# Performance work log

Measured on AMD Instinct MI355X. Metric: run time of the kernel, lower is better.

The kernel has to match this reference:

```python
import jax, jax.numpy as jnp
import numpy as np

N_NODES = 100000
N_EDGES = 800000
F_IN = 128
H1, C1 = 8, 32
N_CLS = 40
NEG_SLOPE = 0.2


def setup_inputs() -> dict:
    key = jax.random.key(0)
    ks = jax.random.split(key, 10)
    s = 1.0 / np.sqrt(F_IN)
    s2 = 1.0 / np.sqrt(H1 * C1)
    return {
        "x": jax.random.normal(ks[0], (N_NODES, F_IN), jnp.float32),
        "edge_index": jax.random.randint(ks[1], (2, N_EDGES), 0, N_NODES, jnp.int64),
        "W1": jax.random.normal(ks[2], (F_IN, H1 * C1), jnp.float32) * s,
        "a_src1": jax.random.normal(ks[3], (H1, C1), jnp.float32) * s2,
        "a_dst1": jax.random.normal(ks[4], (H1, C1), jnp.float32) * s2,
        "b1": jnp.zeros((H1 * C1,), jnp.float32),
        "W2": jax.random.normal(ks[5], (H1 * C1, N_CLS), jnp.float32) * s2,
        "a_src2": jax.random.normal(ks[6], (1, N_CLS), jnp.float32) * 0.1,
        "a_dst2": jax.random.normal(ks[7], (1, N_CLS), jnp.float32) * 0.1,
        "b2": jnp.zeros((N_CLS,), jnp.float32),
    }


def gat_conv(x, src, dst, W, a_src, a_dst, b, heads, out_ch, concat):
    n = x.shape[0]
    h = (x @ W).reshape(n, heads, out_ch)            # [N,H,C]
    alpha_s = jnp.einsum("nhc,hc->nh", h, a_src)     # [N,H]
    alpha_d = jnp.einsum("nhc,hc->nh", h, a_dst)
    e = alpha_s[src] + alpha_d[dst]                  # [E,H]
    e = jax.nn.leaky_relu(e, NEG_SLOPE)
    # per-destination segment softmax (stable)
    m = jax.ops.segment_max(e, dst, num_segments=n)  # [N,H]
    e = jnp.exp(e - m[dst])
    denom = jax.ops.segment_sum(e, dst, num_segments=n)
    alpha = e / (denom[dst] + 1e-16)                 # [E,H]
    msg = alpha[:, :, None] * h[src]                 # [E,H,C]
    out = jax.ops.segment_sum(msg, dst, num_segments=n)  # [N,H,C]
    out = out.reshape(n, heads * out_ch) if concat else out.mean(axis=1)
    return out + b


def reference(x, edge_index, W1, a_src1, a_dst1, b1, W2, a_src2, a_dst2, b2):
    n = x.shape[0]
    # PyG GATConv default add_self_loops=True
    loop = jnp.arange(n, dtype=edge_index.dtype)
    src = jnp.concatenate([edge_index[0], loop])
    dst = jnp.concatenate([edge_index[1], loop])
    # dropout layers are identity in eval mode
    h = gat_conv(x, src, dst, W1, a_src1, a_dst1, b1, H1, C1, concat=True)
    h = jax.nn.elu(h)
    out = gat_conv(h, src, dst, W2, a_src2, a_dst2, b2, 1, N_CLS, concat=False)
    return jax.nn.log_softmax(out, axis=1)
```

## Files before the change

kernel.cpp:

```cpp
#include <hip/hip_runtime.h>
#include <hip/hip_fp16.h>
#include <math.h>

#define N_NODESc 100000
#define N_EDGESc 800000
#define F_INc    128
#define HC1c     256
#define NCLSc    40
#define NEG_SLOPEc 0.2f
#define CAPc     40
#define CSH      4

typedef _Float16 half8 __attribute__((ext_vector_type(8)));
typedef __fp16   f16x2 __attribute__((ext_vector_type(2)));
typedef float    f32x4 __attribute__((ext_vector_type(4)));
typedef float    f32x2 __attribute__((ext_vector_type(2)));

__device__ __forceinline__ unsigned pack_ws(float w, int src) {
    union { f16x2 h; unsigned u; } t;
    t.h = __builtin_amdgcn_cvt_pkrtz(w, w);
    return (unsigned)src | ((t.u & 0xFFFFu) << 17);
}
__device__ __forceinline__ float unpack_w(unsigned pe) {
    union { unsigned short s; __fp16 h; } t;
    t.s = (unsigned short)(pe >> 17);
    return (float)t.h;
}


__global__ void k_init(const float* __restrict__ W1, const float* __restrict__ W2,
                       _Float16* __restrict__ W1Tf, _Float16* __restrict__ W2Tf,
                       int* __restrict__ cnt) {
    if (blockIdx.x < 22) {
        int f = blockIdx.x * 256 + threadIdx.x;
        if (f < 4096) {
            int lane16 = f & 15, quad = (f >> 4) & 3, k0 = (f >> 6) & 3, jt = f >> 8;
            int c = lane16 * 16 + jt;
            int kbase = k0 * 32 + quad * 8;
            _Float16* o = W1Tf + (size_t)f * 8;
            #pragma unroll
            for (int j = 0; j < 8; j++) o[j] = (_Float16)W1[(kbase + j) * HC1c + c];
        } else if (f < 4096 + 1536) {
            int g = f - 4096;
            int lane16 = g & 15, quad = (g >> 4) & 3, k0 = (g >> 6) & 7, jt = g >> 9;
            int c = jt * 16 + lane16;
            int kbase = k0 * 32 + quad * 8;
            _Float16* o = W2Tf + (size_t)g * 8;
            #pragma unroll
            for (int j = 0; j < 8; j++)
                o[j] = (c < NCLSc) ? (_Float16)W2[(kbase + j) * NCLSc + c] : (_Float16)0.f;
        }
    } else {
        int i = (blockIdx.x - 22) * 256 + threadIdx.x;
        if (i < N_NODESc * 4) ((int4*)cnt)[i] = (int4){0, 0, 0, 0};
    }
}


__global__ __launch_bounds__(256) void k_gemm1_scatter(
    const float* __restrict__ x, const _Float16* __restrict__ W1Tf,
    const float* __restrict__ a_src1, const float* __restrict__ a_dst1,
    unsigned char* __restrict__ h1f8, float* __restrict__ as1, float* __restrict__ ad1,
    const int* __restrict__ src, const int* __restrict__ dst,
    int* __restrict__ cnt, int* __restrict__ bucket) {
    if ((blockIdx.x & 1) == 0) {
        int i = (blockIdx.x >> 1) * 256 + threadIdx.x;
        if (i < N_EDGESc / 4) {
            int4 s = ((const int4*)src)[i];
            int4 d = ((const int4*)dst)[i];
            int p0 = atomicAdd(&cnt[d.x << CSH], 1);
            if (p0 < CAPc) __builtin_nontemporal_store(s.x, &bucket[d.x * CAPc + p0]);
            int p1 = atomicAdd(&cnt[d.y << CSH], 1);
            if (p1 < CAPc) __builtin_nontemporal_store(s.y, &bucket[d.y * CAPc + p1]);
            int p2 = atomicAdd(&cnt[d.z << CSH], 1);
            if (p2 < CAPc) __builtin_nontemporal_store(s.z, &bucket[d.z * CAPc + p2]);
            int p3 = atomicAdd(&cnt[d.w << CSH], 1);
            if (p3 < CAPc) __builtin_nontemporal_store(s.w, &bucket[d.w * CAPc + p3]);
        }
        return;
    }
    int wave = ((blockIdx.x >> 1) * 256 + threadIdx.x) >> 6;
    int n0 = wave * 16;
    if (n0 >= N_NODESc) return;
    int L = threadIdx.x & 63, lane16 = L & 15, quad = L >> 4;
    f32x4 acc[16];
    #pragma unroll
    for (int jt = 0; jt < 16; jt++) acc[jt] = (f32x4){0.f, 0.f, 0.f, 0.f};
    const float* A = x + (size_t)(n0 + lane16) * F_INc + quad * 8;
    const _Float16* Bf = W1Tf + L * 8;
    #pragma unroll
    for (int k0 = 0; k0 < 4; k0++) {
        float4 f0 = *(const float4*)(A + k0 * 32);
        float4 f1 = *(const float4*)(A + k0 * 32 + 4);
        union { half8 v; f16x2 h[4]; } af;
        af.h[0] = __builtin_amdgcn_cvt_pkrtz(f0.x, f0.y);
        af.h[1] = __builtin_amdgcn_cvt_pkrtz(f0.z, f0.w);
        af.h[2] = __builtin_amdgcn_cvt_pkrtz(f1.x, f1.y);
        af.h[3] = __builtin_amdgcn_cvt_pkrtz(f1.z, f1.w);
        #pragma unroll
        for (int jt = 0; jt < 16; jt++) {
            half8 bf = *(const half8*)(Bf + (jt * 4 + k0) * 512);
            acc[jt] = __builtin_amdgcn_mfma_f32_16x16x32_f16(af.v, bf, acc[jt], 0, 0, 0);
        }
    }
    {
        #pragma unroll
        for (int r = 0; r < 4; r++) {
            uint4 st;
            int d;
            d = __builtin_amdgcn_cvt_pk_fp8_f32(acc[0][r], acc[1][r], 0, false);
            d = __builtin_amdgcn_cvt_pk_fp8_f32(acc[2][r], acc[3][r], d, true);
            st.x = (unsigned)d;
            d = __builtin_amdgcn_cvt_pk_fp8_f32(acc[4][r], acc[5][r], 0, false);
            d = __builtin_amdgcn_cvt_pk_fp8_f32(acc[6][r], acc[7][r], d, true);
            st.y = (unsigned)d;
            d = __builtin_amdgcn_cvt_pk_fp8_f32(acc[8][r], acc[9][r], 0, false);
            d = __builtin_amdgcn_cvt_pk_fp8_f32(acc[10][r], acc[11][r], d, true);
            st.z = (unsigned)d;
            d = __builtin_amdgcn_cvt_pk_fp8_f32(acc[12][r], acc[13][r], 0, false);
            d = __builtin_amdgcn_cvt_pk_fp8_f32(acc[14][r], acc[15][r], d, true);
            st.w = (unsigned)d;
            *(uint4*)(h1f8 + (size_t)(n0 + quad * 4 + r) * HC1c + lane16 * 16) = st;
        }
    }
    {
        float asv[16], adv[16];
        const float4* ap = (const float4*)(a_src1 + lane16 * 16);
        const float4* dp = (const float4*)(a_dst1 + lane16 * 16);
        #pragma unroll
        for (int q = 0; q < 4; q++) {
            float4 a4 = ap[q], d4 = dp[q];
            asv[4*q] = a4.x; asv[4*q+1] = a4.y; asv[4*q+2] = a4.z; asv[4*q+3] = a4.w;
            adv[4*q] = d4.x; adv[4*q+1] = d4.y; adv[4*q+2] = d4.z; adv[4*q+3] = d4.w;
        }
        float ps[4] = {0,0,0,0}, pd[4] = {0,0,0,0};
        #pragma unroll
        for (int jt = 0; jt < 16; jt++) {
            #pragma unroll
            for (int r = 0; r < 4; r++) {
                ps[r] += acc[jt][r] * asv[jt];
                pd[r] += acc[jt][r] * adv[jt];
            }
        }
        #pragma unroll
        for (int r = 0; r < 4; r++) {
            ps[r] += __shfl_xor(ps[r], 1);
            pd[r] += __shfl_xor(pd[r], 1);
        }
        if ((lane16 & 1) == 0) {
            int h = lane16 >> 1;
            #pragma unroll
            for (int r = 0; r < 4; r++) {
                int n = n0 + quad * 4 + r;
                as1[n * 8 + h] = ps[r];
                ad1[n * 8 + h] = pd[r];
            }
        }
    }
}


__global__ __launch_bounds__(256) void k_agg1(
    const int* __restrict__ cnt, const int* __restrict__ bucket,
    const float* __restrict__ as1, const float* __restrict__ ad1,
    const unsigned char* __restrict__ h1f8, const float* __restrict__ b1,
    _Float16* __restrict__ act1b) {
    int n = blockIdx.x * 4 + (threadIdx.x >> 6);
    if (n >= N_NODESc) return;
    int L = threadIdx.x & 63;
    int eL = L >> 3, hL = L & 7;
    int hA = L >> 3;
    int beg = n * CAPc;
    int end = beg + min(cnt[n << CSH], CAPc);
    float ad = ad1[n * 8 + hL];
    float vs = as1[n * 8 + hL] + ad;
    float s_self = (vs > 0.f) ? vs : NEG_SLOPEc * vs;
    float m_run = s_self, d_run = 1.f;
    unsigned ldself = *((const unsigned*)(h1f8 + (size_t)n * HC1c) + L);
    f32x2 accA = __builtin_amdgcn_cvt_pk_f32_fp8((int)ldself, false);
    f32x2 accB = __builtin_amdgcn_cvt_pk_f32_fp8((int)ldself, true);
    for (int base = beg; base < end; base += 16) {
        int m = min(16, end - base);
        int src0 = 0, src1 = 0;
        float s0 = -INFINITY, s1 = -INFINITY;
        if (eL < m) {
            src0 = bucket[base + eL];
            float v = as1[src0 * 8 + hL] + ad;
            s0 = (v > 0.f) ? v : NEG_SLOPEc * v;
        }
        if (eL + 8 < m) {
            src1 = bucket[base + eL + 8];
            float v = as1[src1 * 8 + hL] + ad;
            s1 = (v > 0.f) ? v : NEG_SLOPEc * v;
        }
        float mc = fmaxf(s0, s1);
        mc = fmaxf(mc, __shfl_xor(mc, 8));
        mc = fmaxf(mc, __shfl_xor(mc, 16));
        mc = fmaxf(mc, __shfl_xor(mc, 32));
        float mnew = fmaxf(m_run, mc);
        float w0 = (eL < m) ? __expf(s0 - mnew) : 0.f;
        float w1 = (eL + 8 < m) ? __expf(s1 - mnew) : 0.f;
        float wsum = w0 + w1;
        wsum += __shfl_xor(wsum, 8);
        wsum += __shfl_xor(wsum, 16);
        wsum += __shfl_xor(wsum, 32);
        float scale = __expf(m_run - mnew);
        d_run = d_run * scale + wsum;
        m_run = mnew;
        float sc = __shfl(scale, hA);
        f32x2 sc2 = (f32x2){sc, sc};
        accA *= sc2;
        accB *= sc2;
        unsigned pk0 = pack_ws(w0, src0);
        unsigned pk1 = pack_ws(w1, src1);
        #pragma unroll
        for (int r = 0; r < 4; r++) {
            int e0 = r * 4;
            if (e0 < m) {
                unsigned pk = (e0 < 8) ? pk0 : pk1;
                unsigned pe[4]; unsigned ld[4];
                #pragma unroll
                for (int j = 0; j < 4; j++)
                    pe[j] = __shfl(pk, ((e0 + j) & 7) * 8 + hA);
                #pragma unroll
                for (int j = 0; j < 4; j++)
                    ld[j] = *((const unsigned*)(h1f8 + (size_t)(pe[j] & 0x1FFFFu) * HC1c) + L);
                #pragma unroll
                for (int j = 0; j < 4; j++) {
                    float w = unpack_w(pe[j]);
                    f32x2 wv = (f32x2){w, w};
                    f32x2 lo = __builtin_amdgcn_cvt_pk_f32_fp8((int)ld[j], false);
                    f32x2 hi = __builtin_amdgcn_cvt_pk_f32_fp8((int)ld[j], true);
                    asm("v_pk_fma_f32 %0, %1, %2, %0" : "+v"(accA) : "v"(wv), "v"(lo));
                    asm("v_pk_fma_f32 %0, %1, %2, %0" : "+v"(accB) : "v"(wv), "v"(hi));
                }
            }
        }
    }
    float inv = __builtin_amdgcn_rcpf(d_run + 1e-16f);
    float inv_h = __shfl(inv, hA);
    float4 bb = ((const float4*)b1)[L];
    float o0 = accA[0] * inv_h + bb.x;
    float o1 = accA[1] * inv_h + bb.y;
    float o2 = accB[0] * inv_h + bb.z;
    float o3 = accB[1] * inv_h + bb.w;
    o0 = (o0 > 0.f) ? o0 : (__expf(o0) - 1.f);
    o1 = (o1 > 0.f) ? o1 : (__expf(o1) - 1.f);
    o2 = (o2 > 0.f) ? o2 : (__expf(o2) - 1.f);
    o3 = (o3 > 0.f) ? o3 : (__expf(o3) - 1.f);
    union { uint2 u; f16x2 h[2]; } st;
    st.h[0] = __builtin_amdgcn_cvt_pkrtz(o0, o1);
    st.h[1] = __builtin_amdgcn_cvt_pkrtz(o2, o3);
    ((uint2*)(act1b + (size_t)n * HC1c))[L] = st.u;
}


__global__ __launch_bounds__(256) void k_gemm2(
    const _Float16* __restrict__ act1b, const _Float16* __restrict__ W2Tf,
    const float* __restrict__ a_src2, const float* __restrict__ a_dst2,
    _Float16* __restrict__ h2b, float* __restrict__ as2, float* __restrict__ ad2) {
    int wave = (blockIdx.x * 256 + threadIdx.x) >> 6;
    int n0 = wave * 16;
    if (n0 >= N_NODESc) return;
    int L = threadIdx.x & 63, lane16 = L & 15, quad = L >> 4;
    f32x4 acc[3];
    #pragma unroll
    for (int jt = 0; jt < 3; jt++) acc[jt] = (f32x4){0.f, 0.f, 0.f, 0.f};
    const _Float16* A = act1b + (size_t)(n0 + lane16) * HC1c + quad * 8;
    const _Float16* Bf = W2Tf + L * 8;
    #pragma unroll
    for (int k0 = 0; k0 < 8; k0++) {
        half8 af = *(const half8*)(A + k0 * 32);
        #pragma unroll
        for (int jt = 0; jt < 3; jt++) {
            half8 bf = *(const half8*)(Bf + (jt * 8 + k0) * 512);
            acc[jt] = __builtin_amdgcn_mfma_f32_16x16x32_f16(af, bf, acc[jt], 0, 0, 0);
        }
    }
    float ps[4] = {0.f, 0.f, 0.f, 0.f}, pd[4] = {0.f, 0.f, 0.f, 0.f};
    #pragma unroll
    for (int jt = 0; jt < 3; jt++) {
        int col = jt * 16 + lane16;
        float ws = (col < NCLSc) ? a_src2[col] : 0.f;
        float wd = (col < NCLSc) ? a_dst2[col] : 0.f;
        #pragma unroll
        for (int r = 0; r < 4; r++) {
            float v = acc[jt][r];
            int n = n0 + quad * 4 + r;
            if (col < NCLSc) h2b[(size_t)n * NCLSc + col] = (_Float16)v;
            ps[r] += v * ws; pd[r] += v * wd;
        }
    }
    #pragma unroll
    for (int r = 0; r < 4; r++) {
        float s = ps[r], d = pd[r];
        s += __shfl_xor(s, 1); d += __shfl_xor(d, 1);
        s += __shfl_xor(s, 2); d += __shfl_xor(d, 2);
        s += __shfl_xor(s, 4); d += __shfl_xor(d, 4);
        s += __shfl_xor(s, 8); d += __shfl_xor(d, 8);
        if (lane16 == 0) {
            int n = n0 + quad * 4 + r;
            as2[n] = s; ad2[n] = d;
        }
    }
}


__global__ __launch_bounds__(256) void k_agg2(
    const int* __restrict__ cnt, const int* __restrict__ bucket,
    const float* __restrict__ as2, const float* __restrict__ ad2,
    const _Float16* __restrict__ h2b, const float* __restrict__ b2,
    float* __restrict__ out) {
    int n = blockIdx.x * 4 + (threadIdx.x >> 6);
    if (n >= N_NODESc) return;
    int L = threadIdx.x & 63;
    int g = L / 20, cls = L % 20;
    int beg = n * CAPc;
    int end = beg + min(cnt[n << CSH], CAPc);
    float ad = ad2[n];
    float vs = as2[n] + ad;
    float s_self = (vs > 0.f) ? vs : NEG_SLOPEc * vs;
    float m_run = s_self, d_run = 1.f;
    f16x2 acc2 = (f16x2){(__fp16)0.f, (__fp16)0.f};
    if (g == 0) {
        union { unsigned u; f16x2 h; } pk;
        pk.u = *((const unsigned*)(h2b + (size_t)n * NCLSc) + cls);
        acc2 = pk.h;
    }
    for (int base = beg; base < end; base += 64) {
        int m = min(64, end - base);
        int src = 0; float s = -INFINITY;
        if (L < m) {
            src = bucket[base + L];
            float v = as2[src] + ad;
            s = (v > 0.f) ? v : NEG_SLOPEc * v;
        }
        float mc = s;
        for (int o = 32; o; o >>= 1) mc = fmaxf(mc, __shfl_xor(mc, o));
        float mnew = fmaxf(m_run, mc);
        float w = (L < m) ? __expf(s - mnew) : 0.f;
        float ws = w;
        for (int o = 32; o; o >>= 1) ws += __shfl_xor(ws, o);
        float scale = __expf(m_run - mnew);
        d_run = d_run * scale + ws;
        m_run = mnew;
        f16x2 sc2 = __builtin_amdgcn_cvt_pkrtz(scale, scale);
        acc2 *= sc2;
        for (int jb = 0; jb < m; jb += 9) {
            float wv[3]; int sev[3]; unsigned ldv[3];
            #pragma unroll
            for (int r = 0; r < 3; r++) {
                int e = jb + r * 3 + g;
                int lane = (e < 64) ? e : 63;
                wv[r] = __shfl(w, lane);
                sev[r] = __shfl(src, lane);
            }
            #pragma unroll
            for (int r = 0; r < 3; r++) {
                ldv[r] = 0u;
                if (g < 3)
                    ldv[r] = *((const unsigned*)(h2b + (size_t)sev[r] * NCLSc) + cls);
            }
            #pragma unroll
            for (int r = 0; r < 3; r++) {
                f16x2 we2 = __builtin_amdgcn_cvt_pkrtz(wv[r], wv[r]);
                union { unsigned u; f16x2 h; } pk; pk.u = ldv[r];
                acc2 += we2 * pk.h;
            }
        }
    }
    union { f16x2 h; int i; } au; au.h = acc2;
    int i1 = __shfl(au.i, (L + 20) & 63);
    int i2 = __shfl(au.i, (L + 40) & 63);
    union { int i; f16x2 h; } b1u, b2u; b1u.i = i1; b2u.i = i2;
    acc2 = acc2 + b1u.h + b2u.h;
    float vx = -INFINITY, vy = -INFINITY;
    if (L < 20) {
        float2 bb = ((const float2*)b2)[L];
        float inv = __builtin_amdgcn_rcpf(d_run + 1e-16f);
        vx = (float)acc2[0] * inv + bb.x;
        vy = (float)acc2[1] * inv + bb.y;
    }
    float mv = fmaxf(vx, vy);
    for (int o = 32; o; o >>= 1) mv = fmaxf(mv, __shfl_xor(mv, o));
    float ex = (L < 20) ? __expf(vx - mv) + __expf(vy - mv) : 0.f;
    for (int o = 32; o; o >>= 1) ex += __shfl_xor(ex, o);
    float ls = __logf(ex);
    if (L < 20) {
        float2 o2; o2.x = vx - mv - ls; o2.y = vy - mv - ls;
        ((float2*)(out + (size_t)n * NCLSc))[L] = o2;
    }
}


extern "C" void kernel_launch(void* const* d_in, const int* in_sizes, int n_in,
                              void* d_out, int out_size, void* d_ws, size_t ws_size,
                              hipStream_t stream) {
    const float* x    = (const float*)d_in[0];
    const int*   ei   = (const int*)d_in[1];
    const float* W1   = (const float*)d_in[2];
    const float* as1w = (const float*)d_in[3];
    const float* ad1w = (const float*)d_in[4];
    const float* b1   = (const float*)d_in[5];
    const float* W2   = (const float*)d_in[6];
    const float* as2w = (const float*)d_in[7];
    const float* ad2w = (const float*)d_in[8];
    const float* b2   = (const float*)d_in[9];
    float* out = (float*)d_out;

    char* p = (char*)d_ws;
    unsigned char* h1f8 = (unsigned char*)p; p += (size_t)N_NODESc * HC1c;
    _Float16* act1b = (_Float16*)p; p += (size_t)N_NODESc * HC1c * 2;
    _Float16* W1Tf  = (_Float16*)p; p += (size_t)4096 * 8 * 2;
    _Float16* W2Tf  = (_Float16*)p; p += (size_t)1536 * 8 * 2;
    float* a_s1 = (float*)p; p += (size_t)N_NODESc * 8 * 4;
    float* a_d1 = (float*)p; p += (size_t)N_NODESc * 8 * 4;
    _Float16* h2b = (_Float16*)p; p += (size_t)N_NODESc * NCLSc * 2;
    float* a_s2 = (float*)p; p += (size_t)N_NODESc * 4;
    float* a_d2 = (float*)p; p += (size_t)N_NODESc * 4;
    int* cnt    = (int*)p;   p += (size_t)N_NODESc * 16 * 4;
    int* bucket = (int*)p;   p += (size_t)N_NODESc * CAPc * 4;
    (void)ws_size; (void)in_sizes; (void)n_in; (void)out_size;

    const int* src = ei;
    const int* dst = ei + N_EDGESc;

    k_init<<<22 + (N_NODESc * 4 + 255) / 256, 256, 0, stream>>>(W1, W2, W1Tf, W2Tf, cnt);

    int nwave_blk = ((N_NODESc + 15) / 16 + 3) / 4;
    k_gemm1_scatter<<<nwave_blk * 2, 256, 0, stream>>>(
        x, W1Tf, as1w, ad1w, h1f8, a_s1, a_d1, src, dst, cnt, bucket);

    k_agg1<<<(N_NODESc + 3) / 4, 256, 0, stream>>>(cnt, bucket, a_s1, a_d1, h1f8, b1, act1b);
    k_gemm2<<<nwave_blk, 256, 0, stream>>>(act1b, W2Tf, as2w, ad2w, h2b, a_s2, a_d2);
    k_agg2<<<(N_NODESc + 3) / 4, 256, 0, stream>>>(cnt, bucket, a_s2, a_d2, h2b, b2, out);
}
```

Baseline: 292.8 us.

## Fuse layer-1 aggregation with layer-2 GEMM through shared memory and interleave scatter blocks

Merges the layer-1 aggregation kernel and the layer-2 GEMM kernel. Each block aggregates 16 nodes (4 per wave), writes the ELU activations as fp16 into swizzled LDS, and then one wave runs the MFMA GEMM against W2. This removes the 51 MB fp16 act1b round trip through global memory and one kernel launch, at the cost of idle waves during the GEMM phase and a block-wide barrier. The gemm1/scatter kernel also changes its block mapping from alternating single blocks to groups of 8, which alters how edge-scatter and GEMM work are interleaved.

Result: slower. 301.0 us (+2.8%).

```diff
diff --git a/kernel.cpp b/kernel.cpp
--- a/kernel.cpp
+++ b/kernel.cpp
@@ -63,8 +63,10 @@
     unsigned char* __restrict__ h1f8, float* __restrict__ as1, float* __restrict__ ad1,
     const int* __restrict__ src, const int* __restrict__ dst,
     int* __restrict__ cnt, int* __restrict__ bucket) {
-    if ((blockIdx.x & 1) == 0) {
-        int i = (blockIdx.x >> 1) * 256 + threadIdx.x;
+    int grp = blockIdx.x >> 3, within = blockIdx.x & 7;
+    if ((grp & 1) == 0) {
+        int sb = (grp >> 1) * 8 + within;
+        int i = sb * 256 + threadIdx.x;
         if (i < N_EDGESc / 4) {
             int4 s = ((const int4*)src)[i];
             int4 d = ((const int4*)dst)[i];
@@ -79,7 +81,8 @@
         }
         return;
     }
-    int wave = ((blockIdx.x >> 1) * 256 + threadIdx.x) >> 6;
+    int gb = (grp >> 1) * 8 + within;
+    int wave = (gb * 256 + (int)threadIdx.x) >> 6;
     int n0 = wave * 16;
     if (n0 >= N_NODESc) return;
     int L = threadIdx.x & 63, lane16 = L & 15, quad = L >> 4;
@@ -160,147 +163,150 @@
 }
 
 
-__global__ __launch_bounds__(256) void k_agg1(
+__global__ __launch_bounds__(256) void k_agg1_g2(
     const int* __restrict__ cnt, const int* __restrict__ bucket,
     const float* __restrict__ as1, const float* __restrict__ ad1,
     const unsigned char* __restrict__ h1f8, const float* __restrict__ b1,
-    _Float16* __restrict__ act1b) {
-    int n = blockIdx.x * 4 + (threadIdx.x >> 6);
-    if (n >= N_NODESc) return;
+    const _Float16* __restrict__ W2Tf, const float* __restrict__ a_src2,
+    const float* __restrict__ a_dst2, _Float16* __restrict__ h2b,
+    float* __restrict__ as2, float* __restrict__ ad2) {
+    __shared__ _Float16 sact[16 * HC1c];
     int L = threadIdx.x & 63;
+    int wid = threadIdx.x >> 6;
     int eL = L >> 3, hL = L & 7;
     int hA = L >> 3;
-    int beg = n * CAPc;
-    int end = beg + min(cnt[n << CSH], CAPc);
-    float ad = ad1[n * 8 + hL];
-    float vs = as1[n * 8 + hL] + ad;
-    float s_self = (vs > 0.f) ? vs : NEG_SLOPEc * vs;
-    float m_run = s_self, d_run = 1.f;
-    unsigned ldself = *((const unsigned*)(h1f8 + (size_t)n * HC1c) + L);
-    f32x2 accA = __builtin_amdgcn_cvt_pk_f32_fp8((int)ldself, false);
-    f32x2 accB = __builtin_amdgcn_cvt_pk_f32_fp8((int)ldself, true);
-    for (int base = beg; base < end; base += 16) {
-        int m = min(16, end - base);
-        int src0 = 0, src1 = 0;
-        float s0 = -INFINITY, s1 = -INFINITY;
-        if (eL < m) {
-            src0 = bucket[base + eL];
-            float v = as1[src0 * 8 + hL] + ad;
-            s0 = (v > 0.f) ? v : NEG_SLOPEc * v;
-        }
-        if (eL + 8 < m) {
-            src1 = bucket[base + eL + 8];
-            float v = as1[src1 * 8 + hL] + ad;
-            s1 = (v > 0.f) ? v : NEG_SLOPEc * v;
-        }
-        float mc = fmaxf(s0, s1);
-        mc = fmaxf(mc, __shfl_xor(mc, 8));
-        mc = fmaxf(mc, __shfl_xor(mc, 16));
-        mc = fmaxf(mc, __shfl_xor(mc, 32));
-        float mnew = fmaxf(m_run, mc);
-        float w0 = (eL < m) ? __expf(s0 - mnew) : 0.f;
-        float w1 = (eL + 8 < m) ? __expf(s1 - mnew) : 0.f;
-        float wsum = w0 + w1;
-        wsum += __shfl_xor(wsum, 8);
-        wsum += __shfl_xor(wsum, 16);
-        wsum += __shfl_xor(wsum, 32);
-        float scale = __expf(m_run - mnew);
-        d_run = d_run * scale + wsum;
-        m_run = mnew;
-        float sc = __shfl(scale, hA);
-        f32x2 sc2 = (f32x2){sc, sc};
-        accA *= sc2;
-        accB *= sc2;
-        unsigned pk0 = pack_ws(w0, src0);
-        unsigned pk1 = pack_ws(w1, src1);
+    float4 bb = ((const float4*)b1)[L];
+    #pragma unroll 1
+    for (int nn = 0; nn < 4; nn++) {
+        int row = wid * 4 + nn;
+        int n = blockIdx.x * 16 + row;
+        int beg = n * CAPc;
+        int end = beg + min(cnt[n << CSH], CAPc);
+        float ad = ad1[n * 8 + hL];
+        float vs = as1[n * 8 + hL] + ad;
+        float s_self = (vs > 0.f) ? vs : NEG_SLOPEc * vs;
+        float m_run = s_self, d_run = 1.f;
+        unsigned ldself = *((const unsigned*)(h1f8 + (size_t)n * HC1c) + L);
+        f32x2 accA = __builtin_amdgcn_cvt_pk_f32_fp8((int)ldself, false);
+        f32x2 accB = __builtin_amdgcn_cvt_pk_f32_fp8((int)ldself, true);
+        for (int base = beg; base < end; base += 16) {
+            int m = min(16, end - base);
+            int src0 = 0, src1 = 0;
+            float s0 = -INFINITY, s1 = -INFINITY;
+            if (eL < m) {
+                src0 = bucket[base + eL];
+                float v = as1[src0 * 8 + hL] + ad;
+                s0 = (v > 0.f) ? v : NEG_SLOPEc * v;
+            }
+            if (eL + 8 < m) {
+                src1 = bucket[base + eL + 8];
+                float v = as1[src1 * 8 + hL] + ad;
+                s1 = (v > 0.f) ? v : NEG_SLOPEc * v;
+            }
+            float mc = fmaxf(s0, s1);
+            mc = fmaxf(mc, __shfl_xor(mc, 8));
+            mc = fmaxf(mc, __shfl_xor(mc, 16));
+            mc = fmaxf(mc, __shfl_xor(mc, 32));
+            float mnew = fmaxf(m_run, mc);
+            float w0 = (eL < m) ? __expf(s0 - mnew) : 0.f;
+            float w1 = (eL + 8 < m) ? __expf(s1 - mnew) : 0.f;
+            float wsum = w0 + w1;
+            wsum += __shfl_xor(wsum, 8);
+            wsum += __shfl_xor(wsum, 16);
+            wsum += __shfl_xor(wsum, 32);
+            float scale = __expf(m_run - mnew);
+            d_run = d_run * scale + wsum;
+            m_run = mnew;
+            float sc = __shfl(scale, hA);
+            f32x2 sc2 = (f32x2){sc, sc};
+            accA *= sc2;
+            accB *= sc2;
+            unsigned pk0 = pack_ws(w0, src0);
+            unsigned pk1 = pack_ws(w1, src1);
+            #pragma unroll
+            for (int r = 0; r < 4; r++) {
+                int e0 = r * 4;
+                if (e0 < m) {
+                    unsigned pk = (e0 < 8) ? pk0 : pk1;
+                    unsigned pe[4]; unsigned ld[4];
+                    #pragma unroll
+                    for (int j = 0; j < 4; j++)
+                        pe[j] = __shfl(pk, ((e0 + j) & 7) * 8 + hA);
+                    #pragma unroll
+                    for (int j = 0; j < 4; j++)
+                        ld[j] = *((const unsigned*)(h1f8 + (size_t)(pe[j] & 0x1FFFFu) * HC1c) + L);
+                    #pragma unroll
+                    for (int j = 0; j < 4; j++) {
+                        float w = unpack_w(pe[j]);
+                        f32x2 wv = (f32x2){w, w};
+                        f32x2 lo = __builtin_amdgcn_cvt_pk_f32_fp8((int)ld[j], false);
+                        f32x2 hi = __builtin_amdgcn_cvt_pk_f32_fp8((int)ld[j], true);
+                        asm("v_pk_fma_f32 %0, %1, %2, %0" : "+v"(accA) : "v"(wv), "v"(lo));
+                        asm("v_pk_fma_f32 %0, %1, %2, %0" : "+v"(accB) : "v"(wv), "v"(hi));
+                    }
+                }
+            }
+        }
+        float inv = __builtin_amdgcn_rcpf(d_run + 1e-16f);
+        float inv_h = __shfl(inv, hA);
+        float o0 = accA[0] * inv_h + bb.x;
+        float o1 = accA[1] * inv_h + bb.y;
+        float o2 = accB[0] * inv_h + bb.z;
+        float o3 = accB[1] * inv_h + bb.w;
+        o0 = (o0 > 0.f) ? o0 : (__expf(o0) - 1.f);
+        o1 = (o1 > 0.f) ? o1 : (__expf(o1) - 1.f);
+        o2 = (o2 > 0.f) ? o2 : (__expf(o2) - 1.f);
+        o3 = (o3 > 0.f) ? o3 : (__expf(o3) - 1.f);
+        union { uint2 u; f16x2 h[2]; } st;
+        st.h[0] = __builtin_amdgcn_cvt_pkrtz(o0, o1);
+        st.h[1] = __builtin_amdgcn_cvt_pkrtz(o2, o3);
+        unsigned bofs = ((unsigned)(row * 512 + L * 8)) ^ ((unsigned)(row & 7) << 4);
+        *(uint2*)((char*)sact + bofs) = st.u;
+    }
+    __syncthreads();
+    if (threadIdx.x < 64) {
+        int lane16 = L & 15, quad = L >> 4;
+        int n0 = blockIdx.x * 16;
+        f32x4 acc[3];
+        #pragma unroll
+        for (int jt = 0; jt < 3; jt++) acc[jt] = (f32x4){0.f, 0.f, 0.f, 0.f};
+        const _Float16* Bf = W2Tf + L * 8;
+        unsigned rmask = ((unsigned)(lane16 & 7) << 4);
+        #pragma unroll
+        for (int k0 = 0; k0 < 8; k0++) {
+            unsigned abofs = ((unsigned)(lane16 * 512 + quad * 16 + k0 * 64)) ^ rmask;
+            half8 af = *(const half8*)((const char*)sact + abofs);
+            #pragma unroll
+            for (int jt = 0; jt < 3; jt++) {
+                half8 bf = *(const half8*)(Bf + (jt * 8 + k0) * 512);
+                acc[jt] = __builtin_amdgcn_mfma_f32_16x16x32_f16(af, bf, acc[jt], 0, 0, 0);
+            }
+        }
+        float ps[4] = {0.f, 0.f, 0.f, 0.f}, pd[4] = {0.f, 0.f, 0.f, 0.f};
+        #pragma unroll
+        for (int jt = 0; jt < 3; jt++) {
+            int col = jt * 16 + lane16;
+            float ws = (col < NCLSc) ? a_src2[col] : 0.f;
+            float wd = (col < NCLSc) ? a_dst2[col] : 0.f;
+            #pragma unroll
+            for (int r = 0; r < 4; r++) {
+                float v = acc[jt][r];
+                int n = n0 + quad * 4 + r;
+                if (col < NCLSc) h2b[(size_t)n * NCLSc + col] = (_Float16)v;
+                ps[r] += v * ws; pd[r] += v * wd;
+            }
+        }
         #pragma unroll
         for (int r = 0; r < 4; r++) {
-            int e0 = r * 4;
-            if (e0 < m) {
-                unsigned pk = (e0 < 8) ? pk0 : pk1;
-                unsigned pe[4]; unsigned ld[4];
-                #pragma unroll
-                for (int j = 0; j < 4; j++)
-                    pe[j] = __shfl(pk, ((e0 + j) & 7) * 8 + hA);
-                #pragma unroll
-                for (int j = 0; j < 4; j++)
-                    ld[j] = *((const unsigned*)(h1f8 + (size_t)(pe[j] & 0x1FFFFu) * HC1c) + L);
-                #pragma unroll
-                for (int j = 0; j < 4; j++) {
-                    float w = unpack_w(pe[j]);
-                    f32x2 wv = (f32x2){w, w};
-                    f32x2 lo = __builtin_amdgcn_cvt_pk_f32_fp8((int)ld[j], false);
-                    f32x2 hi = __builtin_amdgcn_cvt_pk_f32_fp8((int)ld[j], true);
-                    asm("v_pk_fma_f32 %0, %1, %2, %0" : "+v"(accA) : "v"(wv), "v"(lo));
-                    asm("v_pk_fma_f32 %0, %1, %2, %0" : "+v"(accB) : "v"(wv), "v"(hi));
-                }
-            }
-        }
-    }
-    float inv = __builtin_amdgcn_rcpf(d_run + 1e-16f);
-    float inv_h = __shfl(inv, hA);
-    float4 bb = ((const float4*)b1)[L];
-    float o0 = accA[0] * inv_h + bb.x;
-    float o1 = accA[1] * inv_h + bb.y;
-    float o2 = accB[0] * inv_h + bb.z;
-    float o3 = accB[1] * inv_h + bb.w;
-    o0 = (o0 > 0.f) ? o0 : (__expf(o0) - 1.f);
-    o1 = (o1 > 0.f) ? o1 : (__expf(o1) - 1.f);
-    o2 = (o2 > 0.f) ? o2 : (__expf(o2) - 1.f);
-    o3 = (o3 > 0.f) ? o3 : (__expf(o3) - 1.f);
-    union { uint2 u; f16x2 h[2]; } st;
-    st.h[0] = __builtin_amdgcn_cvt_pkrtz(o0, o1);
-    st.h[1] = __builtin_amdgcn_cvt_pkrtz(o2, o3);
-    ((uint2*)(act1b + (size_t)n * HC1c))[L] = st.u;
-}
-
-
-__global__ __launch_bounds__(256) void k_gemm2(
-    const _Float16* __restrict__ act1b, const _Float16* __restrict__ W2Tf,
-    const float* __restrict__ a_src2, const float* __restrict__ a_dst2,
-    _Float16* __restrict__ h2b, float* __restrict__ as2, float* __restrict__ ad2) {
-    int wave = (blockIdx.x * 256 + threadIdx.x) >> 6;
-    int n0 = wave * 16;
-    if (n0 >= N_NODESc) return;
-    int L = threadIdx.x & 63, lane16 = L & 15, quad = L >> 4;
-    f32x4 acc[3];
-    #pragma unroll
-    for (int jt = 0; jt < 3; jt++) acc[jt] = (f32x4){0.f, 0.f, 0.f, 0.f};
-    const _Float16* A = act1b + (size_t)(n0 + lane16) * HC1c + quad * 8;
-    const _Float16* Bf = W2Tf + L * 8;
-    #pragma unroll
-    for (int k0 = 0; k0 < 8; k0++) {
-        half8 af = *(const half8*)(A + k0 * 32);
-        #pragma unroll
-        for (int jt = 0; jt < 3; jt++) {
-            half8 bf = *(const half8*)(Bf + (jt * 8 + k0) * 512);
-            acc[jt] = __builtin_amdgcn_mfma_f32_16x16x32_f16(af, bf, acc[jt], 0, 0, 0);
-        }
-    }
-    float ps[4] = {0.f, 0.f, 0.f, 0.f}, pd[4] = {0.f, 0.f, 0.f, 0.f};
-    #pragma unroll
-    for (int jt = 0; jt < 3; jt++) {
-        int col = jt * 16 + lane16;
-        float ws = (col < NCLSc) ? a_src2[col] : 0.f;
-        float wd = (col < NCLSc) ? a_dst2[col] : 0.f;
-        #pragma unroll
-        for (int r = 0; r < 4; r++) {
-            float v = acc[jt][r];
-            int n = n0 + quad * 4 + r;
-            if (col < NCLSc) h2b[(size_t)n * NCLSc + col] = (_Float16)v;
-            ps[r] += v * ws; pd[r] += v * wd;
-        }
-    }
-    #pragma unroll
-    for (int r = 0; r < 4; r++) {
-        float s = ps[r], d = pd[r];
-        s += __shfl_xor(s, 1); d += __shfl_xor(d, 1);
-        s += __shfl_xor(s, 2); d += __shfl_xor(d, 2);
-        s += __shfl_xor(s, 4); d += __shfl_xor(d, 4);
-        s += __shfl_xor(s, 8); d += __shfl_xor(d, 8);
-        if (lane16 == 0) {
-            int n = n0 + quad * 4 + r;
-            as2[n] = s; ad2[n] = d;
+            float s = ps[r], d = pd[r];
+            s += __shfl_xor(s, 1); d += __shfl_xor(d, 1);
+            s += __shfl_xor(s, 2); d += __shfl_xor(d, 2);
+            s += __shfl_xor(s, 4); d += __shfl_xor(d, 4);
+            s += __shfl_xor(s, 8); d += __shfl_xor(d, 8);
+            if (lane16 == 0) {
+                int n = n0 + quad * 4 + r;
+                as2[n] = s; ad2[n] = d;
+            }
         }
     }
 }
@@ -410,7 +416,6 @@
 
     char* p = (char*)d_ws;
     unsigned char* h1f8 = (unsigned char*)p; p += (size_t)N_NODESc * HC1c;
-    _Float16* act1b = (_Float16*)p; p += (size_t)N_NODESc * HC1c * 2;
     _Float16* W1Tf  = (_Float16*)p; p += (size_t)4096 * 8 * 2;
     _Float16* W2Tf  = (_Float16*)p; p += (size_t)1536 * 8 * 2;
     float* a_s1 = (float*)p; p += (size_t)N_NODESc * 8 * 4;
@@ -427,11 +432,11 @@
 
     k_init<<<22 + (N_NODESc * 4 + 255) / 256, 256, 0, stream>>>(W1, W2, W1Tf, W2Tf, cnt);
 
-    int nwave_blk = ((N_NODESc + 15) / 16 + 3) / 4;
-    k_gemm1_scatter<<<nwave_blk * 2, 256, 0, stream>>>(
+    k_gemm1_scatter<<<3136, 256, 0, stream>>>(
         x, W1Tf, as1w, ad1w, h1f8, a_s1, a_d1, src, dst, cnt, bucket);
 
-    k_agg1<<<(N_NODESc + 3) / 4, 256, 0, stream>>>(cnt, bucket, a_s1, a_d1, h1f8, b1, act1b);
-    k_gemm2<<<nwave_blk, 256, 0, stream>>>(act1b, W2Tf, as2w, ad2w, h2b, a_s2, a_d2);
+    k_agg1_g2<<<N_NODESc / 16, 256, 0, stream>>>(
+        cnt, bucket, a_s1, a_d1, h1f8, b1, W2Tf, as2w, ad2w, h2b, a_s2, a_d2);
+
     k_agg2<<<(N_NODESc + 3) / 4, 256, 0, stream>>>(cnt, bucket, a_s2, a_d2, h2b, b2, out);
 }
```

## Process two destination nodes per wave in layer-2 aggregation

Applied to the files above, without the earlier changes.

The layer-2 aggregation kernel now gives each 64-lane wave two destination nodes, one per 32-lane half, instead of one node split into three 20-lane edge groups. Reductions shrink to 32-lane shuffles, the final cross-group combine goes away, and the grid is halved. The scatter phase also issues all four atomics before the bucket stores so their latencies overlap. Per-node edge parallelism drops from three edges per step to one (unrolled by three), which could lengthen the dependent load chain on high-degree nodes.

New measurement: 280.1 us. -4.4%, faster.

```diff
diff --git a/kernel.cpp b/kernel.cpp
--- a/kernel.cpp
+++ b/kernel.cpp
@@ -69,17 +69,17 @@
             int4 s = ((const int4*)src)[i];
             int4 d = ((const int4*)dst)[i];
             int p0 = atomicAdd(&cnt[d.x << CSH], 1);
+            int p1 = atomicAdd(&cnt[d.y << CSH], 1);
+            int p2 = atomicAdd(&cnt[d.z << CSH], 1);
+            int p3 = atomicAdd(&cnt[d.w << CSH], 1);
             if (p0 < CAPc) __builtin_nontemporal_store(s.x, &bucket[d.x * CAPc + p0]);
-            int p1 = atomicAdd(&cnt[d.y << CSH], 1);
             if (p1 < CAPc) __builtin_nontemporal_store(s.y, &bucket[d.y * CAPc + p1]);
-            int p2 = atomicAdd(&cnt[d.z << CSH], 1);
             if (p2 < CAPc) __builtin_nontemporal_store(s.z, &bucket[d.z * CAPc + p2]);
-            int p3 = atomicAdd(&cnt[d.w << CSH], 1);
             if (p3 < CAPc) __builtin_nontemporal_store(s.w, &bucket[d.w * CAPc + p3]);
         }
         return;
     }
-    int wave = ((blockIdx.x >> 1) * 256 + threadIdx.x) >> 6;
+    int wave = ((blockIdx.x >> 1) * 256 + (int)threadIdx.x) >> 6;
     int n0 = wave * 16;
     if (n0 >= N_NODESc) return;
     int L = threadIdx.x & 63, lane16 = L & 15, quad = L >> 4;
@@ -311,10 +311,9 @@
     const float* __restrict__ as2, const float* __restrict__ ad2,
     const _Float16* __restrict__ h2b, const float* __restrict__ b2,
     float* __restrict__ out) {
-    int n = blockIdx.x * 4 + (threadIdx.x >> 6);
-    if (n >= N_NODESc) return;
     int L = threadIdx.x & 63;
-    int g = L / 20, cls = L % 20;
+    int half = L >> 5, l32 = L & 31;
+    int n = blockIdx.x * 8 + (int)(threadIdx.x >> 6) * 2 + half;
     int beg = n * CAPc;
     int end = beg + min(cnt[n << CSH], CAPc);
     float ad = ad2[n];
@@ -322,44 +321,47 @@
     float s_self = (vs > 0.f) ? vs : NEG_SLOPEc * vs;
     float m_run = s_self, d_run = 1.f;
     f16x2 acc2 = (f16x2){(__fp16)0.f, (__fp16)0.f};
-    if (g == 0) {
+    if (l32 < 20) {
         union { unsigned u; f16x2 h; } pk;
-        pk.u = *((const unsigned*)(h2b + (size_t)n * NCLSc) + cls);
+        pk.u = *((const unsigned*)(h2b + (size_t)n * NCLSc) + l32);
         acc2 = pk.h;
     }
-    for (int base = beg; base < end; base += 64) {
-        int m = min(64, end - base);
+    for (int base = beg; base < end; base += 32) {
+        int m = min(32, end - base);
         int src = 0; float s = -INFINITY;
-        if (L < m) {
-            src = bucket[base + L];
+        if (l32 < m) {
+            src = bucket[base + l32];
             float v = as2[src] + ad;
             s = (v > 0.f) ? v : NEG_SLOPEc * v;
         }
         float mc = s;
-        for (int o = 32; o; o >>= 1) mc = fmaxf(mc, __shfl_xor(mc, o));
+        #pragma unroll
+        for (int o = 16; o; o >>= 1) mc = fmaxf(mc, __shfl_xor(mc, o));
         float mnew = fmaxf(m_run, mc);
-        float w = (L < m) ? __expf(s - mnew) : 0.f;
+        float w = (l32 < m) ? __expf(s - mnew) : 0.f;
         float ws = w;
-        for (int o = 32; o; o >>= 1) ws += __shfl_xor(ws, o);
+        #pragma unroll
+        for (int o = 16; o; o >>= 1) ws += __shfl_xor(ws, o);
         float scale = __expf(m_run - mnew);
         d_run = d_run * scale + ws;
         m_run = mnew;
         f16x2 sc2 = __builtin_amdgcn_cvt_pkrtz(scale, scale);
         acc2 *= sc2;
-        for (int jb = 0; jb < m; jb += 9) {
+        for (int jb = 0; jb < m; jb += 3) {
             float wv[3]; int sev[3]; unsigned ldv[3];
             #pragma unroll
             for (int r = 0; r < 3; r++) {
-                int e = jb + r * 3 + g;
-                int lane = (e < 64) ? e : 63;
+                int e = jb + r;
+                int lane = half * 32 + (e & 31);
                 wv[r] = __shfl(w, lane);
                 sev[r] = __shfl(src, lane);
+                if (e >= m) wv[r] = 0.f;
             }
             #pragma unroll
             for (int r = 0; r < 3; r++) {
                 ldv[r] = 0u;
-                if (g < 3)
-                    ldv[r] = *((const unsigned*)(h2b + (size_t)sev[r] * NCLSc) + cls);
+                if (l32 < 20)
+                    ldv[r] = *((const unsigned*)(h2b + (size_t)sev[r] * NCLSc) + l32);
             }
             #pragma unroll
             for (int r = 0; r < 3; r++) {
@@ -369,26 +371,23 @@
             }
         }
     }
-    union { f16x2 h; int i; } au; au.h = acc2;
-    int i1 = __shfl(au.i, (L + 20) & 63);
-    int i2 = __shfl(au.i, (L + 40) & 63);
-    union { int i; f16x2 h; } b1u, b2u; b1u.i = i1; b2u.i = i2;
-    acc2 = acc2 + b1u.h + b2u.h;
     float vx = -INFINITY, vy = -INFINITY;
-    if (L < 20) {
-        float2 bb = ((const float2*)b2)[L];
+    if (l32 < 20) {
+        float2 bb = ((const float2*)b2)[l32];
         float inv = __builtin_amdgcn_rcpf(d_run + 1e-16f);
         vx = (float)acc2[0] * inv + bb.x;
         vy = (float)acc2[1] * inv + bb.y;
     }
     float mv = fmaxf(vx, vy);
-    for (int o = 32; o; o >>= 1) mv = fmaxf(mv, __shfl_xor(mv, o));
-    float ex = (L < 20) ? __expf(vx - mv) + __expf(vy - mv) : 0.f;
-    for (int o = 32; o; o >>= 1) ex += __shfl_xor(ex, o);
+    #pragma unroll
+    for (int o = 16; o; o >>= 1) mv = fmaxf(mv, __shfl_xor(mv, o));
+    float ex = (l32 < 20) ? __expf(vx - mv) + __expf(vy - mv) : 0.f;
+    #pragma unroll
+    for (int o = 16; o; o >>= 1) ex += __shfl_xor(ex, o);
     float ls = __logf(ex);
-    if (L < 20) {
+    if (l32 < 20) {
         float2 o2; o2.x = vx - mv - ls; o2.y = vy - mv - ls;
-        ((float2*)(out + (size_t)n * NCLSc))[L] = o2;
+        ((float2*)(out + (size_t)n * NCLSc))[l32] = o2;
     }
 }
 
@@ -433,5 +432,5 @@
 
     k_agg1<<<(N_NODESc + 3) / 4, 256, 0, stream>>>(cnt, bucket, a_s1, a_d1, h1f8, b1, act1b);
     k_gemm2<<<nwave_blk, 256, 0, stream>>>(act1b, W2Tf, as2w, ad2w, h2b, a_s2, a_d2);
-    k_agg2<<<(N_NODESc + 3) / 4, 256, 0, stream>>>(cnt, bucket, a_s2, a_d2, h2b, b2, out);
-}
+    k_agg2<<<N_NODESc / 8, 256, 0, stream>>>(cnt, bucket, a_s2, a_d2, h2b, b2, out);
+}
```
